# Performance work log

Measured on AMD Instinct MI355X. Metric: run time of the kernel, lower is better.

The kernel has to match this reference:

```python
import jax, jax.numpy as jnp
import numpy as np

Q, D, DIM, VOCAB = 4096, 32768, 128, 32000


def setup_inputs() -> dict:
    key = jax.random.key(0)
    k1, k2, k3, k4, k5, k6 = jax.random.split(key, 6)
    return {
        "query_embeddings": jax.random.normal(k1, (Q, DIM), dtype=jnp.float32),
        "doc_embeddings": jax.random.normal(k2, (D, DIM), dtype=jnp.float32),
        "query_token_ids": jax.random.randint(k3, (Q,), 0, VOCAB, dtype=jnp.int32),
        "doc_token_ids": jax.random.randint(k4, (D,), 0, VOCAB, dtype=jnp.int32),
        "query_weight_table": jax.random.uniform(k5, (VOCAB,), dtype=jnp.float32),
        "doc_weight_table": jax.random.uniform(k6, (VOCAB,), dtype=jnp.float32),
    }


def reference(query_embeddings, doc_embeddings, query_token_ids, doc_token_ids,
              query_weight_table, doc_weight_table):
    # token-level MaxSim: [Q, D] similarity, max over doc tokens
    sim = jnp.einsum('qd,kd->qk', query_embeddings, doc_embeddings)  # [Q, D]
    max_sim = jnp.max(sim, axis=1)          # [Q]
    max_idx = jnp.argmax(sim, axis=1)       # [Q]

    # token_weighter: learned scalar weight per token id
    query_weights = query_weight_table[query_token_ids]             # [Q]
    best_doc_ids = doc_token_ids[max_idx]                           # [Q] device-side gather
    doc_weights = doc_weight_table[best_doc_ids]                    # [Q]

    combined = query_weights * doc_weights                          # [Q]
    # 'linear' normalization with zero-sum fallback to uniform weights
    wsum = jnp.sum(combined)
    safe = jnp.where(wsum > 0, wsum, jnp.float32(1.0))
    uniform = jnp.full_like(combined, 1.0 / combined.shape[0])
    normalized = jnp.where(wsum > 0, combined / safe, uniform)

    return jnp.sum(max_sim * normalized)
```

## Files before the change

kernel.cpp:

```cpp
#include <hip/hip_runtime.h>
#include <hip/hip_bf16.h>
#include <stdint.h>

#define Q_N   4096
#define D_N   32768
#define DIM   128
#define VOCAB 32000

#define NCHUNK 16
#define CHUNK  (D_N / NCHUNK)
#define QTILE  128
#define DSUB   128
#define NSLOT  (NCHUNK * 2)

typedef short  short8 __attribute__((ext_vector_type(8)));
typedef float  f32x4  __attribute__((ext_vector_type(4)));

#define WS_QBF  0u
#define WS_DBF  0x100000u
#define WS_PMAX 0x900000u
#define WS_PIDX 0x980000u
#define WS_SUMS 0xA00000u

__device__ inline ushort f2bf(float f) {
  uint32_t u = __float_as_uint(f);
  u += 0x7FFFu + ((u >> 16) & 1u);
  return (ushort)(u >> 16);
}

__global__ void convert_kernel(const float* __restrict__ qe, const float* __restrict__ de,
                               ushort* __restrict__ qb, ushort* __restrict__ db,
                               float* __restrict__ sums) {
  int i = blockIdx.x * 256 + threadIdx.x;
  if (i < 3) sums[i] = 0.0f;
  const int NQ4 = Q_N * DIM / 4;
  float4 v;
  ushort* dst;
  if (i < NQ4) {
    v = ((const float4*)qe)[i];
    dst = qb + (size_t)i * 4;
  } else {
    int j = i - NQ4;
    v = ((const float4*)de)[j];
    dst = db + (size_t)j * 4;
  }
  ushort4 o;
  o.x = f2bf(v.x); o.y = f2bf(v.y); o.z = f2bf(v.z); o.w = f2bf(v.w);
  *(ushort4*)dst = o;
}

__global__ __launch_bounds__(512, 4)
void maxsim_kernel(const ushort* __restrict__ dbf, const ushort* __restrict__ qbf,
                   float* __restrict__ pmax, int* __restrict__ pidx) {
  __shared__ ushort lds[2][DSUB * DIM];

  const int tid  = threadIdx.x;
  const int lane = tid & 63;
  const int wid  = tid >> 6;
  const int wm   = wid >> 2;
  const int wn   = wid & 3;
  const int qblock = blockIdx.x * QTILE;
  const int chunk0 = blockIdx.y * CHUNK;

  short8 bfr[2][4];
  #pragma unroll
  for (int nf = 0; nf < 2; ++nf) {
    int qrow = qblock + wn * 32 + nf * 16 + (lane & 15);
    const ushort* p = qbf + (size_t)qrow * DIM + ((lane >> 4) * 8);
    #pragma unroll
    for (int kk = 0; kk < 4; ++kk)
      bfr[nf][kk] = *(const short8*)(p + kk * 32);
  }

  float rmax[2]; int ridx[2];
  #pragma unroll
  for (int nf = 0; nf < 2; ++nf) { rmax[nf] = -3.0e38f; ridx[nf] = 0; }

  const char* gdoc = (const char*)(dbf + (size_t)chunk0 * DIM);

  auto stage = [&](int b, int st) {
    const char* gt = gdoc + st * (DSUB * DIM * 2);
    char* lb = (char*)&lds[b][0];
    #pragma unroll
    for (int it = 0; it < 4; ++it) {
      int off = wid * 4096 + it * 1024 + lane * 16;
      int swz = off ^ (((off >> 8) & 7) << 4);
      __builtin_amdgcn_global_load_lds(
          (const __attribute__((address_space(1))) uint32_t*)(gt + swz),
          (__attribute__((address_space(3))) uint32_t*)(lb + wid * 4096 + it * 1024),
          16, 0, 0);
    }
  };

  stage(0, 0);
  __syncthreads();

  #pragma unroll 1
  for (int st = 0; st < CHUNK / DSUB; ++st) {
    const int b = st & 1;
    if (st + 1 < CHUNK / DSUB) stage(b ^ 1, st + 1);

    const char* lb = (const char*)&lds[b][0];
    #pragma unroll
    for (int mf = 0; mf < 4; ++mf) {
      short8 afr[4];
      int arow = wm * 64 + mf * 16 + (lane & 15);
      #pragma unroll
      for (int kk = 0; kk < 4; ++kk) {
        int abyte = (arow * 256 + kk * 64 + ((lane >> 4) * 16)) ^ ((arow & 7) << 4);
        afr[kk] = *(const short8*)(lb + abyte);
      }
      f32x4 acc[2] = {{0.f,0.f,0.f,0.f},{0.f,0.f,0.f,0.f}};
      #pragma unroll
      for (int kk = 0; kk < 4; ++kk)
        #pragma unroll
        for (int nf = 0; nf < 2; ++nf)
          acc[nf] = __builtin_amdgcn_mfma_f32_16x16x32_bf16(afr[kk], bfr[nf][kk], acc[nf], 0, 0, 0);
      const int code0 = st * 128 + wm * 64 + mf * 16;
      #pragma unroll
      for (int nf = 0; nf < 2; ++nf)
        #pragma unroll
        for (int r = 0; r < 4; ++r) {
          float v = acc[nf][r];
          bool gtv = v > rmax[nf];
          rmax[nf] = gtv ? v : rmax[nf];
          ridx[nf] = gtv ? (code0 + r) : ridx[nf];
        }
    }
    __syncthreads();
  }

  const int slot = blockIdx.y * 2 + wm;
  #pragma unroll
  for (int nf = 0; nf < 2; ++nf) {
    float m = rmax[nf];
    int gi = chunk0 + ridx[nf] + ((lane >> 4) << 2);
    #pragma unroll
    for (int s = 16; s <= 32; s <<= 1) {
      float om = __shfl_xor(m, s);
      int   oi = __shfl_xor(gi, s);
      if (om > m || (om == m && oi < gi)) { m = om; gi = oi; }
    }
    if (lane < 16) {
      int q = qblock + wn * 32 + nf * 16 + lane;
      pmax[slot * Q_N + q] = m;
      pidx[slot * Q_N + q] = gi;
    }
  }
}

__global__ void reduce_kernel(const float* __restrict__ pmax, const int* __restrict__ pidx,
                              const int* __restrict__ qtok, const int* __restrict__ dtok,
                              const float* __restrict__ qwt, const float* __restrict__ dwt,
                              float* __restrict__ sums) {
  int q = blockIdx.x * 256 + threadIdx.x;
  float m = -3.0e38f; int best = 0;
  #pragma unroll 4
  for (int s = 0; s < NSLOT; ++s) {
    float v = pmax[s * Q_N + q];
    int   i = pidx[s * Q_N + q];
    if (v > m || (v == m && i < best)) { m = v; best = i; }
  }
  float c  = qwt[qtok[q]] * dwt[dtok[best]];
  float s0 = c, s1 = m * c, s2 = m;
  #pragma unroll
  for (int sh = 32; sh >= 1; sh >>= 1) {
    s0 += __shfl_down(s0, sh);
    s1 += __shfl_down(s1, sh);
    s2 += __shfl_down(s2, sh);
  }
  __shared__ float red[3][4];
  int lane = threadIdx.x & 63, w = threadIdx.x >> 6;
  if (lane == 0) { red[0][w] = s0; red[1][w] = s1; red[2][w] = s2; }
  __syncthreads();
  if (threadIdx.x == 0) {
    atomicAdd(&sums[0], red[0][0] + red[0][1] + red[0][2] + red[0][3]);
    atomicAdd(&sums[1], red[1][0] + red[1][1] + red[1][2] + red[1][3]);
    atomicAdd(&sums[2], red[2][0] + red[2][1] + red[2][2] + red[2][3]);
  }
}

__global__ void finalize_kernel(const float* __restrict__ sums, float* __restrict__ out) {
  float s0 = sums[0], s1 = sums[1], s2 = sums[2];
  out[0] = (s0 > 0.0f) ? (s1 / s0) : (s2 / (float)Q_N);
}

extern "C" void kernel_launch(void* const* d_in, const int* in_sizes, int n_in,
                              void* d_out, int out_size, void* d_ws, size_t ws_size,
                              hipStream_t stream) {
  const float* qe   = (const float*)d_in[0];
  const float* de   = (const float*)d_in[1];
  const int*   qtok = (const int*)d_in[2];
  const int*   dtok = (const int*)d_in[3];
  const float* qwt  = (const float*)d_in[4];
  const float* dwt  = (const float*)d_in[5];
  float* out = (float*)d_out;

  char* ws = (char*)d_ws;
  ushort* qbf  = (ushort*)(ws + WS_QBF);
  ushort* dbf  = (ushort*)(ws + WS_DBF);
  float*  pmax = (float*)(ws + WS_PMAX);
  int*    pidx = (int*)(ws + WS_PIDX);
  float*  sums = (float*)(ws + WS_SUMS);

  const int NQ4 = Q_N * DIM / 4, ND4 = D_N * DIM / 4;
  convert_kernel<<<(NQ4 + ND4) / 256, 256, 0, stream>>>(qe, de, qbf, dbf, sums);

  dim3 g(Q_N / QTILE, NCHUNK);
  maxsim_kernel<<<g, 512, 0, stream>>>(dbf, qbf, pmax, pidx);

  reduce_kernel<<<Q_N / 256, 256, 0, stream>>>(pmax, pidx, qtok, dtok, qwt, dwt, sums);
  finalize_kernel<<<1, 1, 0, stream>>>(sums, out);
}
```

Before: 127.0 us.

## Widen query tile to 256, remap blocks per XCD, pack partial max/index

Each block now covers 256 queries, with four 16-wide query fragments per wave, so every doc tile staged in LDS feeds twice as many MFMAs. The doc dimension is split into 32 chunks, and a 1D grid maps blocks so each XCD works on the same doc chunks, to improve L2 reuse. Partial max and argmax are stored as one interleaved float2 array for coalesced reads in the reduce kernel, and swizzled staging offsets are precomputed once. The cost is more registers for the query fragments and accumulators, which may lower occupancy under the 512x4 launch bound, and twice as many partial slots to reduce.

Result: slower. 139.0 us (+9.4%).

```diff
diff --git a/kernel.cpp b/kernel.cpp
--- a/kernel.cpp
+++ b/kernel.cpp
@@ -7,10 +7,12 @@
 #define DIM   128
 #define VOCAB 32000
 
-#define NCHUNK 16
+#define NCHUNK 32
 #define CHUNK  (D_N / NCHUNK)
-#define QTILE  128
+#define QTILE  256
+#define NQT    (Q_N / QTILE)
 #define DSUB   128
+#define NSUB   (CHUNK / DSUB)
 #define NSLOT  (NCHUNK * 2)
 
 typedef short  short8 __attribute__((ext_vector_type(8)));
@@ -18,9 +20,8 @@
 
 #define WS_QBF  0u
 #define WS_DBF  0x100000u
-#define WS_PMAX 0x900000u
-#define WS_PIDX 0x980000u
-#define WS_SUMS 0xA00000u
+#define WS_PMI  0x900000u
+#define WS_SUMS 0xB00000u
 
 __device__ inline ushort f2bf(float f) {
   uint32_t u = __float_as_uint(f);
@@ -32,7 +33,7 @@
                                ushort* __restrict__ qb, ushort* __restrict__ db,
                                float* __restrict__ sums) {
   int i = blockIdx.x * 256 + threadIdx.x;
-  if (i < 3) sums[i] = 0.0f;
+  if (i < 4) sums[i] = 0.0f;
   const int NQ4 = Q_N * DIM / 4;
   float4 v;
   ushort* dst;
@@ -51,7 +52,7 @@
 
 __global__ __launch_bounds__(512, 4)
 void maxsim_kernel(const ushort* __restrict__ dbf, const ushort* __restrict__ qbf,
-                   float* __restrict__ pmax, int* __restrict__ pidx) {
+                   float2* __restrict__ pmi) {
   __shared__ ushort lds[2][DSUB * DIM];
 
   const int tid  = threadIdx.x;
@@ -59,35 +60,46 @@
   const int wid  = tid >> 6;
   const int wm   = wid >> 2;
   const int wn   = wid & 3;
-  const int qblock = blockIdx.x * QTILE;
-  const int chunk0 = blockIdx.y * CHUNK;
-
-  short8 bfr[2][4];
-  #pragma unroll
-  for (int nf = 0; nf < 2; ++nf) {
-    int qrow = qblock + wn * 32 + nf * 16 + (lane & 15);
+
+  const int bid  = blockIdx.x;
+  const int xcd  = bid & 7;
+  const int slot = bid >> 3;
+  const int c    = xcd + 8 * (slot >> 4);
+  const int qt   = slot & 15;
+  const int qblock = qt * QTILE;
+  const int chunk0 = c * CHUNK;
+
+  short8 bfr[4][4];
+  #pragma unroll
+  for (int nf = 0; nf < 4; ++nf) {
+    int qrow = qblock + wn * 64 + nf * 16 + (lane & 15);
     const ushort* p = qbf + (size_t)qrow * DIM + ((lane >> 4) * 8);
     #pragma unroll
     for (int kk = 0; kk < 4; ++kk)
       bfr[nf][kk] = *(const short8*)(p + kk * 32);
   }
 
-  float rmax[2]; int ridx[2];
-  #pragma unroll
-  for (int nf = 0; nf < 2; ++nf) { rmax[nf] = -3.0e38f; ridx[nf] = 0; }
+  float rmax[4]; int ridx[4];
+  #pragma unroll
+  for (int nf = 0; nf < 4; ++nf) { rmax[nf] = -3.0e38f; ridx[nf] = 0; }
 
   const char* gdoc = (const char*)(dbf + (size_t)chunk0 * DIM);
+
+  int swzoff[4];
+  #pragma unroll
+  for (int it = 0; it < 4; ++it) {
+    int o = wid * 4096 + it * 1024 + lane * 16;
+    swzoff[it] = o ^ (((o >> 8) & 7) << 4);
+  }
 
   auto stage = [&](int b, int st) {
     const char* gt = gdoc + st * (DSUB * DIM * 2);
-    char* lb = (char*)&lds[b][0];
+    char* lb = (char*)&lds[b][0] + wid * 4096;
     #pragma unroll
     for (int it = 0; it < 4; ++it) {
-      int off = wid * 4096 + it * 1024 + lane * 16;
-      int swz = off ^ (((off >> 8) & 7) << 4);
       __builtin_amdgcn_global_load_lds(
-          (const __attribute__((address_space(1))) uint32_t*)(gt + swz),
-          (__attribute__((address_space(3))) uint32_t*)(lb + wid * 4096 + it * 1024),
+          (const __attribute__((address_space(1))) uint32_t*)(gt + swzoff[it]),
+          (__attribute__((address_space(3))) uint32_t*)(lb + it * 1024),
           16, 0, 0);
     }
   };
@@ -96,9 +108,9 @@
   __syncthreads();
 
   #pragma unroll 1
-  for (int st = 0; st < CHUNK / DSUB; ++st) {
+  for (int st = 0; st < NSUB; ++st) {
     const int b = st & 1;
-    if (st + 1 < CHUNK / DSUB) stage(b ^ 1, st + 1);
+    if (st + 1 < NSUB) stage(b ^ 1, st + 1);
 
     const char* lb = (const char*)&lds[b][0];
     #pragma unroll
@@ -110,15 +122,17 @@
         int abyte = (arow * 256 + kk * 64 + ((lane >> 4) * 16)) ^ ((arow & 7) << 4);
         afr[kk] = *(const short8*)(lb + abyte);
       }
-      f32x4 acc[2] = {{0.f,0.f,0.f,0.f},{0.f,0.f,0.f,0.f}};
+      f32x4 acc[4];
+      #pragma unroll
+      for (int nf = 0; nf < 4; ++nf) acc[nf] = (f32x4){0.f, 0.f, 0.f, 0.f};
       #pragma unroll
       for (int kk = 0; kk < 4; ++kk)
         #pragma unroll
-        for (int nf = 0; nf < 2; ++nf)
+        for (int nf = 0; nf < 4; ++nf)
           acc[nf] = __builtin_amdgcn_mfma_f32_16x16x32_bf16(afr[kk], bfr[nf][kk], acc[nf], 0, 0, 0);
       const int code0 = st * 128 + wm * 64 + mf * 16;
       #pragma unroll
-      for (int nf = 0; nf < 2; ++nf)
+      for (int nf = 0; nf < 4; ++nf)
         #pragma unroll
         for (int r = 0; r < 4; ++r) {
           float v = acc[nf][r];
@@ -130,9 +144,9 @@
     __syncthreads();
   }
 
-  const int slot = blockIdx.y * 2 + wm;
-  #pragma unroll
-  for (int nf = 0; nf < 2; ++nf) {
+  const int pslot = c * 2 + wm;
+  #pragma unroll
+  for (int nf = 0; nf < 4; ++nf) {
     float m = rmax[nf];
     int gi = chunk0 + ridx[nf] + ((lane >> 4) << 2);
     #pragma unroll
@@ -142,27 +156,26 @@
       if (om > m || (om == m && oi < gi)) { m = om; gi = oi; }
     }
     if (lane < 16) {
-      int q = qblock + wn * 32 + nf * 16 + lane;
-      pmax[slot * Q_N + q] = m;
-      pidx[slot * Q_N + q] = gi;
-    }
-  }
-}
-
-__global__ void reduce_kernel(const float* __restrict__ pmax, const int* __restrict__ pidx,
+      int q = qblock + wn * 64 + nf * 16 + lane;
+      pmi[pslot * Q_N + q] = make_float2(m, __int_as_float(gi));
+    }
+  }
+}
+
+__global__ void reduce_kernel(const float2* __restrict__ pmi,
                               const int* __restrict__ qtok, const int* __restrict__ dtok,
                               const float* __restrict__ qwt, const float* __restrict__ dwt,
                               float* __restrict__ sums) {
   int q = blockIdx.x * 256 + threadIdx.x;
   float m = -3.0e38f; int best = 0;
-  #pragma unroll 4
+  #pragma unroll 8
   for (int s = 0; s < NSLOT; ++s) {
-    float v = pmax[s * Q_N + q];
-    int   i = pidx[s * Q_N + q];
-    if (v > m || (v == m && i < best)) { m = v; best = i; }
-  }
-  float c  = qwt[qtok[q]] * dwt[dtok[best]];
-  float s0 = c, s1 = m * c, s2 = m;
+    float2 p = pmi[s * Q_N + q];
+    int i = __float_as_int(p.y);
+    if (p.x > m || (p.x == m && i < best)) { m = p.x; best = i; }
+  }
+  float cmb = qwt[qtok[q]] * dwt[dtok[best]];
+  float s0 = cmb, s1 = m * cmb, s2 = m;
   #pragma unroll
   for (int sh = 32; sh >= 1; sh >>= 1) {
     s0 += __shfl_down(s0, sh);
@@ -199,16 +212,14 @@
   char* ws = (char*)d_ws;
   ushort* qbf  = (ushort*)(ws + WS_QBF);
   ushort* dbf  = (ushort*)(ws + WS_DBF);
-  float*  pmax = (float*)(ws + WS_PMAX);
-  int*    pidx = (int*)(ws + WS_PIDX);
+  float2* pmi  = (float2*)(ws + WS_PMI);
   float*  sums = (float*)(ws + WS_SUMS);
 
   const int NQ4 = Q_N * DIM / 4, ND4 = D_N * DIM / 4;
   convert_kernel<<<(NQ4 + ND4) / 256, 256, 0, stream>>>(qe, de, qbf, dbf, sums);
 
-  dim3 g(Q_N / QTILE, NCHUNK);
-  maxsim_kernel<<<g, 512, 0, stream>>>(dbf, qbf, pmax, pidx);
-
-  reduce_kernel<<<Q_N / 256, 256, 0, stream>>>(pmax, pidx, qtok, dtok, qwt, dwt, sums);
+  maxsim_kernel<<<NQT * NCHUNK, 512, 0, stream>>>(dbf, qbf, pmi);
+
+  reduce_kernel<<<Q_N / 256, 256, 0, stream>>>(pmi, qtok, dtok, qwt, dwt, sums);
   finalize_kernel<<<1, 1, 0, stream>>>(sums, out);
 }
```
